# Performance work log

Hardware: AMD Instinct MI355X
Metric: run time of the kernel (lower is better)

## Reference

```python
import jax, jax.numpy as jnp
import numpy as np

B, N = 32, 25200          # batch, anchors (YOLOX @ 1280, strides 8/16/32)
NUM_CLASSES = 80
CH = 5 + NUM_CLASSES
CONF_THRE = 0.7
NMS_THRE = 0.45
TOPK = 512                # fixed pre-/post-NMS candidate budget (jit-static)
CLASS_OFFSET = 4096.0     # class-offset trick from the torch code


def setup_inputs() -> dict:
    key = jax.random.key(0)
    pred = jax.random.uniform(key, (B, N, CH), dtype=jnp.float32)
    # put box coords in pixel scale so IoU/NMS behaves realistically
    pred = pred.at[..., :4].multiply(640.0)
    return {"prediction": pred}


def _pairwise_iou(boxes):
    # boxes: [K, 4] xyxy -> iou: [K, K] (same math as torchvision.ops.nms)
    x1, y1, x2, y2 = boxes[:, 0], boxes[:, 1], boxes[:, 2], boxes[:, 3]
    area = (x2 - x1) * (y2 - y1)
    iw = jnp.clip(jnp.minimum(x2[:, None], x2[None, :]) - jnp.maximum(x1[:, None], x1[None, :]), 0.0)
    ih = jnp.clip(jnp.minimum(y2[:, None], y2[None, :]) - jnp.maximum(y1[:, None], y1[None, :]), 0.0)
    inter = iw * ih
    return inter / (area[:, None] + area[None, :] - inter)


def _greedy_nms(boxes, valid, iou_thre):
    # boxes are pre-sorted by descending score; greedy suppression identical to torchvision NMS
    iou = _pairwise_iou(boxes)  # [K, K]
    idx = jnp.arange(boxes.shape[0])

    def body(i, keep):
        suppress = (iou[i] > iou_thre) & (idx > i) & keep[i]
        return keep & ~suppress

    return jax.lax.fori_loop(0, boxes.shape[0], body, valid)


def _per_image(pred):
    # pred: [N, 5+C]
    cx, cy, w, h = pred[:, 0], pred[:, 1], pred[:, 2], pred[:, 3]
    hw, hh = w * 0.5, h * 0.5
    boxes = jnp.stack([cx - hw, cy - hh, cx + hw, cy + hh], axis=1)  # [N, 4] xyxy

    cls_scores = pred[:, 5:5 + NUM_CLASSES]
    class_conf = jnp.max(cls_scores, axis=1)
    class_pred = jnp.argmax(cls_scores, axis=1)
    conf = pred[:, 4] * class_conf                      # obj * class score
    valid = conf >= CONF_THRE

    # confidence filter + sort-by-score via fixed-size top-k (invalids ranked last)
    rank = jnp.where(valid, conf, -1.0)
    _, order = jax.lax.top_k(rank, TOPK)                # [TOPK], descending score
    b = boxes[order]
    c = conf[order]
    cl = class_pred[order]
    v = valid[order]

    nms_boxes = b + cl.astype(b.dtype)[:, None] * CLASS_OFFSET
    keep = _greedy_nms(nms_boxes, v, NMS_THRE)          # [TOPK] bool

    det = jnp.concatenate([b, c[:, None], cl.astype(jnp.float32)[:, None]], axis=1)  # [TOPK, 6]
    det = det * jax.lax.stop_gradient(keep.astype(det.dtype))[:, None]
    return det, keep


def reference(prediction):
    # returns padded detections [B, TOPK, 6] (x1,y1,x2,y2,conf,cls) and keep mask [B, TOPK]
    det, keep = jax.vmap(_per_image)(prediction)
    return det, keep
```

## Files before the change

kernel.cpp:

```cpp
#include <hip/hip_runtime.h>
#include <stdint.h>

#define BATCH 32
#define NANCH 25200
#define CH 85
#define NCLS 80
#define TOPK 512
#define CONF_THRE 0.7f
#define NMS_THRE 0.45f
#define CLS_OFF 4096.0f

typedef unsigned long long u64;
typedef unsigned int u32;

#define OFF_CONF  0
#define OFF_NMS   3225600
#define OFF_DET   3553280
#define OFF_VALID 3946496
#define OFF_MASK  3948544

__global__ __launch_bounds__(256) void scan_kernel(const float* __restrict__ pred,
                                                   u32* __restrict__ conf32) {
    const int tid = threadIdx.x;
    const int lane = tid & 63;
    const int wv = tid >> 6;
    const int g = lane >> 4;
    const int l = lane & 15;
    const int a = blockIdx.x * 16 + wv * 4 + g;
    const size_t base = (size_t)a * CH;

    float m = -1.0f, obj = 0.0f;
    {
        const float4 q = *(const float4*)(pred + base + (l << 2));
        const int p = l << 2;
        if (p + 0 >= 5) m = fmaxf(m, q.x); else if (p + 0 == 4) obj = q.x;
        if (p + 1 >= 5) m = fmaxf(m, q.y); else if (p + 1 == 4) obj = q.y;
        if (p + 2 >= 5) m = fmaxf(m, q.z); else if (p + 2 == 4) obj = q.z;
        if (p + 3 >= 5) m = fmaxf(m, q.w); else if (p + 3 == 4) obj = q.w;
    }
    if (l < 5) {
        const float4 q = *(const float4*)(pred + base + 64 + (l << 2));
        m = fmaxf(fmaxf(m, fmaxf(q.x, q.y)), fmaxf(q.z, q.w));
    } else if (l == 5) {
        m = fmaxf(m, pred[base + 84]);
    }
    #pragma unroll
    for (int off = 1; off < 16; off <<= 1) m = fmaxf(m, __shfl_xor(m, off));
    const float ob = __shfl(obj, (lane & 48) + 1);
    const float conf = ob * m;
    if (l == 0)
        conf32[a] = (conf >= CONF_THRE) ? __float_as_uint(conf) : 0u;
}

__global__ __launch_bounds__(1024) void select_kernel(const float* __restrict__ pred,
                                                      const u32* __restrict__ conf32,
                                                      float* __restrict__ nmsG,
                                                      float* __restrict__ detG,
                                                      u64* __restrict__ validG) {
    __shared__ u64 sbuf[1024];
    __shared__ u64 sorted[1024];
    __shared__ u32 hist[256];
    __shared__ u32 wtot[4];
    __shared__ u32 s_cnt, s_pivot;
    __shared__ unsigned char val[TOPK];

    const int img = blockIdx.x;
    const int tid = threadIdx.x;
    const int lane = tid & 63;
    const int wv = tid >> 6;

    if (tid == 0) { s_cnt = 0u; s_pivot = 0u; }
    if (tid < 256) hist[tid] = 0u;
    __syncthreads();

    const u32* cd = conf32 + (size_t)img * NANCH;
    for (int i = tid; i < NANCH; i += 1024) {
        const u32 c = cd[i];
        if (c) atomicAdd(&hist[(c >> 15) & 255u], 1u);
    }
    __syncthreads();

    u32 v = 0, s = 0;
    if (tid < 256) {
        v = hist[tid]; s = v;
        #pragma unroll
        for (int off = 1; off < 64; off <<= 1) {
            const u32 t = __shfl_down(s, off);
            if (lane + off < 64) s += t;
        }
        if (lane == 0) wtot[wv] = s;
    }
    __syncthreads();
    if (tid < 256) {
        u32 add = 0;
        for (int w2 = wv + 1; w2 < 4; ++w2) add += wtot[w2];
        const u32 sfull = s + add;
        const u32 snext = sfull - v;
        if (sfull >= TOPK && snext < TOPK) s_pivot = (u32)tid;
    }
    __syncthreads();
    const u32 T = 0x3F000000u | (s_pivot << 15);

    for (int i = tid; i < NANCH; i += 1024) {
        const u32 c = cd[i];
        if (c >= T) {
            const u32 pos = atomicAdd(&s_cnt, 1u);
            if (pos < 1024u)
                sbuf[pos] = ((u64)c << 32) | (u64)(0xFFFFFFFFu - (u32)i);
        }
    }
    __syncthreads();
    const u32 mc = (s_cnt > 1024u) ? 1024u : s_cnt;

    sorted[tid] = 0ull;
    u32 rank = 0; u64 my = 0ull;
    if (tid < (int)mc) {
        my = sbuf[tid];
        for (u32 i = 0; i < mc; ++i) rank += (sbuf[i] > my) ? 1u : 0u;
    }
    __syncthreads();
    if (tid < (int)mc && rank < 1024u) sorted[rank] = my;
    __syncthreads();

    const int g = lane >> 4;
    const int l = lane & 15;
    float* nb_ = nmsG + (size_t)img * (5 * TOPK);
    float* dt_ = detG + (size_t)img * (6 * TOPK);
    for (int pass = 0; pass < 8; ++pass) {
        const int r = pass * 64 + wv * 4 + g;
        const u64 key = sorted[r];
        const float conf = __uint_as_float((u32)(key >> 32));
        const bool okrow = conf >= CONF_THRE;
        float x1 = 0.f, y1 = 0.f, x2 = 0.f, y2 = 0.f, clsf = 0.f;
        float vv = -1.0f;
        int ci = l;
        if (okrow) {
            const u32 anchor = 0xFFFFFFFFu - (u32)(key & 0xFFFFFFFFull);
            const float* row = pred + ((size_t)img * NANCH + anchor) * CH;
            const float v0 = row[5 + l];
            const float v1 = row[21 + l];
            const float v2 = row[37 + l];
            const float v3 = row[53 + l];
            const float v4 = row[69 + l];
            float4 box;
            if (l == 0) box = *(const float4*)row;
            vv = v0; ci = l;
            if (v1 > vv) { vv = v1; ci = 16 + l; }
            if (v2 > vv) { vv = v2; ci = 32 + l; }
            if (v3 > vv) { vv = v3; ci = 48 + l; }
            if (v4 > vv) { vv = v4; ci = 64 + l; }
            #pragma unroll
            for (int off = 8; off > 0; off >>= 1) {
                const float ov = __shfl_xor(vv, off);
                const int oi = __shfl_xor(ci, off);
                if (ov > vv || (ov == vv && oi < ci)) { vv = ov; ci = oi; }
            }
            if (l == 0) {
                const float hw = box.z * 0.5f, hh = box.w * 0.5f;
                x1 = box.x - hw; y1 = box.y - hh; x2 = box.x + hw; y2 = box.y + hh;
                clsf = (float)ci;
            }
        }
        if (l == 0) {
            const float off = clsf * CLS_OFF;
            const float X1 = x1 + off, Y1 = y1 + off, X2 = x2 + off, Y2 = y2 + off;
            nb_[0 * TOPK + r] = X1; nb_[1 * TOPK + r] = Y1;
            nb_[2 * TOPK + r] = X2; nb_[3 * TOPK + r] = Y2;
            nb_[4 * TOPK + r] = (X2 - X1) * (Y2 - Y1);
            dt_[r * 6 + 0] = x1; dt_[r * 6 + 1] = y1;
            dt_[r * 6 + 2] = x2; dt_[r * 6 + 3] = y2;
            dt_[r * 6 + 4] = okrow ? conf : 0.0f;
            dt_[r * 6 + 5] = clsf;
            val[r] = okrow ? 1 : 0;
        }
    }
    __syncthreads();

    if (tid < TOPK) {
        const u64 vb = __ballot(val[tid] != 0);
        if (lane == 0) validG[img * 8 + wv] = vb;
    }
}

__global__ __launch_bounds__(256) void iou_kernel(const float* __restrict__ nmsG,
                                                  u64* __restrict__ maskG) {
    __shared__ float bx1[TOPK], by1[TOPK], bx2[TOPK], by2[TOPK], bar[TOPK];
    const int img = blockIdx.x;
    const int slab = blockIdx.y;
    const int tid = threadIdx.x;
    const int lane = tid & 63;
    const float* nb_ = nmsG + (size_t)img * (5 * TOPK);
    for (int i = tid; i < TOPK; i += 256) {
        bx1[i] = nb_[i];            by1[i] = nb_[TOPK + i];
        bx2[i] = nb_[2 * TOPK + i]; by2[i] = nb_[3 * TOPK + i];
        bar[i] = nb_[4 * TOPK + i];
    }
    __syncthreads();
    const int q0 = slab * (16 * TOPK);
    for (int q = q0 + tid; q < q0 + 16 * TOPK; q += 256) {
        const int i = q >> 9;
        const int j = q & (TOPK - 1);
        bool sup = false;
        if (j > i) {
            const float xx1 = fmaxf(bx1[i], bx1[j]);
            const float yy1 = fmaxf(by1[i], by1[j]);
            const float xx2 = fminf(bx2[i], bx2[j]);
            const float yy2 = fminf(by2[i], by2[j]);
            const float iw = fmaxf(xx2 - xx1, 0.0f);
            const float ih = fmaxf(yy2 - yy1, 0.0f);
            const float inter = iw * ih;
            const float uni = bar[i] + bar[j] - inter;
            const float iou = inter / uni;
            sup = iou > NMS_THRE;
        }
        const u64 bm = __ballot(sup);
        if (lane == 0) maskG[(size_t)img * 4096 + (q >> 6)] = bm;
    }
}

__global__ __launch_bounds__(256) void greedy_kernel(const u64* __restrict__ maskG,
                                                     const u64* __restrict__ validG,
                                                     const float* __restrict__ detG,
                                                     float* __restrict__ out) {
    __shared__ u64 m[TOPK * 8];
    __shared__ u64 kw8[8];
    const int img = blockIdx.x;
    const int tid = threadIdx.x;
    const int lane = tid & 63;
    const int wv = tid >> 6;
    const u64* mg = maskG + (size_t)img * 4096;
    for (int i = tid; i < 4096; i += 256) m[i] = mg[i];
    __syncthreads();

    if (wv == 0) {
        const bool ld = lane < 8;
        u64 kw = ld ? validG[img * 8 + lane] : 0ull;
        u64 p0 = ld ? m[0 * 8 + lane] : 0ull;
        u64 p1 = ld ? m[1 * 8 + lane] : 0ull;
        u64 p2 = ld ? m[2 * 8 + lane] : 0ull;
        u64 p3 = ld ? m[3 * 8 + lane] : 0ull;
        for (int i = 0; i < TOPK; i += 4) {
            {
                const u64 w = __shfl(kw, i >> 6);
                const u64 bit = (w >> (i & 63)) & 1ull;
                kw &= ~(p0 & (0ull - bit));
                p0 = (ld && i + 4 < TOPK) ? m[(i + 4) * 8 + lane] : 0ull;
            }
            {
                const u64 w = __shfl(kw, (i + 1) >> 6);
                const u64 bit = (w >> ((i + 1) & 63)) & 1ull;
                kw &= ~(p1 & (0ull - bit));
                p1 = (ld && i + 5 < TOPK) ? m[(i + 5) * 8 + lane] : 0ull;
            }
            {
                const u64 w = __shfl(kw, (i + 2) >> 6);
                const u64 bit = (w >> ((i + 2) & 63)) & 1ull;
                kw &= ~(p2 & (0ull - bit));
                p2 = (ld && i + 6 < TOPK) ? m[(i + 6) * 8 + lane] : 0ull;
            }
            {
                const u64 w = __shfl(kw, (i + 3) >> 6);
                const u64 bit = (w >> ((i + 3) & 63)) & 1ull;
                kw &= ~(p3 & (0ull - bit));
                p3 = (ld && i + 7 < TOPK) ? m[(i + 7) * 8 + lane] : 0ull;
            }
        }
        if (ld) kw8[lane] = kw;
    }
    __syncthreads();

    const float* dt_ = detG + (size_t)img * (6 * TOPK);
    float* det_out = out + (size_t)img * (TOPK * 6);
    float* keep_out = out + (size_t)BATCH * TOPK * 6 + (size_t)img * TOPK;
    for (int idx = tid; idx < TOPK * 6; idx += 256) {
        const int r = idx / 6;
        const float kf = ((kw8[r >> 6] >> (r & 63)) & 1ull) ? 1.0f : 0.0f;
        det_out[idx] = dt_[idx] * kf;
    }
    for (int r = tid; r < TOPK; r += 256) {
        keep_out[r] = ((kw8[r >> 6] >> (r & 63)) & 1ull) ? 1.0f : 0.0f;
    }
}

extern "C" void kernel_launch(void* const* d_in, const int* in_sizes, int n_in,
                              void* d_out, int out_size, void* d_ws, size_t ws_size,
                              hipStream_t stream) {
    const float* pred = (const float*)d_in[0];
    float* out = (float*)d_out;
    char* ws = (char*)d_ws;
    u32* conf32 = (u32*)(ws + OFF_CONF);
    float* nmsG = (float*)(ws + OFF_NMS);
    float* detG = (float*)(ws + OFF_DET);
    u64* validG = (u64*)(ws + OFF_VALID);
    u64* maskG = (u64*)(ws + OFF_MASK);

    scan_kernel<<<(BATCH * NANCH) / 16, 256, 0, stream>>>(pred, conf32);
    select_kernel<<<BATCH, 1024, 0, stream>>>(pred, conf32, nmsG, detG, validG);
    dim3 g4(BATCH, 32);
    iou_kernel<<<g4, 256, 0, stream>>>(nmsG, maskG);
    greedy_kernel<<<BATCH, 256, 0, stream>>>(maskG, validG, detG, out);
}
```

Measured before the change: 449.2 us.

## Compact passing anchors into per-image lists during scan, narrow class-argmax groups

The scan kernel now appends only the anchors that pass the confidence threshold to a per-image list, using a block-level ballot and one global atomic per block. The select kernel then builds its histogram and collects candidates from that short list instead of rereading all 25200 confidence words twice per image. This cuts the serial per-image work in the single-block select stage. It adds a zero kernel launch, an extra shared-memory barrier and global atomics in the scan, and makes the list order nondeterministic, though ties are still broken by anchor index. The class-argmax gather also moves from 16 lanes per row to 8 lanes per row, handling twice as many rows per pass.

```diff
diff --git a/kernel.cpp b/kernel.cpp
--- a/kernel.cpp
+++ b/kernel.cpp
@@ -13,14 +13,21 @@
 typedef unsigned long long u64;
 typedef unsigned int u32;
 
-#define OFF_CONF  0
-#define OFF_NMS   3225600
-#define OFF_DET   3553280
-#define OFF_VALID 3946496
-#define OFF_MASK  3948544
+#define OFF_LIST  0
+#define OFF_CNT   6451200
+#define OFF_NMS   6451456
+#define OFF_DET   6779136
+#define OFF_VALID 7172352
+#define OFF_MASK  7174400
+
+__global__ __launch_bounds__(64) void zero_kernel(u32* __restrict__ cntG) {
+    if (threadIdx.x < BATCH) cntG[threadIdx.x] = 0u;
+}
 
 __global__ __launch_bounds__(256) void scan_kernel(const float* __restrict__ pred,
-                                                   u32* __restrict__ conf32) {
+                                                   u64* __restrict__ listG,
+                                                   u32* __restrict__ cntG) {
+    __shared__ u32 sc[16];
     const int tid = threadIdx.x;
     const int lane = tid & 63;
     const int wv = tid >> 6;
@@ -49,11 +56,31 @@
     const float ob = __shfl(obj, (lane & 48) + 1);
     const float conf = ob * m;
     if (l == 0)
-        conf32[a] = (conf >= CONF_THRE) ? __float_as_uint(conf) : 0u;
+        sc[wv * 4 + g] = (conf >= CONF_THRE) ? __float_as_uint(conf) : 0u;
+    __syncthreads();
+
+    if (tid < 16) {
+        const u32 cc = sc[tid];
+        const u64 mask = __ballot(cc != 0u);
+        if (mask) {
+            const u32 n = __popc((u32)mask);
+            const u32 img = (u32)blockIdx.x / (NANCH / 16);
+            u32 bs = 0;
+            if (tid == 0) bs = atomicAdd(&cntG[img], n);
+            bs = __shfl(bs, 0);
+            if (cc) {
+                const u32 rnk = __popc((u32)mask & ((1u << tid) - 1u));
+                const u32 anchor = (u32)(blockIdx.x * 16 + tid) - img * NANCH;
+                listG[(size_t)img * NANCH + bs + rnk] =
+                    ((u64)cc << 32) | (u64)(0xFFFFFFFFu - anchor);
+            }
+        }
+    }
 }
 
 __global__ __launch_bounds__(1024) void select_kernel(const float* __restrict__ pred,
-                                                      const u32* __restrict__ conf32,
+                                                      const u64* __restrict__ listG,
+                                                      const u32* __restrict__ cntG,
                                                       float* __restrict__ nmsG,
                                                       float* __restrict__ detG,
                                                       u64* __restrict__ validG) {
@@ -73,10 +100,12 @@
     if (tid < 256) hist[tid] = 0u;
     __syncthreads();
 
-    const u32* cd = conf32 + (size_t)img * NANCH;
-    for (int i = tid; i < NANCH; i += 1024) {
-        const u32 c = cd[i];
-        if (c) atomicAdd(&hist[(c >> 15) & 255u], 1u);
+    const u32 cnt = cntG[img];
+    const u64* keys = listG + (size_t)img * NANCH;
+
+    for (u32 i = tid; i < cnt; i += 1024) {
+        const u32 c = (u32)(keys[i] >> 32);
+        atomicAdd(&hist[(c >> 15) & 255u], 1u);
     }
     __syncthreads();
 
@@ -101,12 +130,11 @@
     __syncthreads();
     const u32 T = 0x3F000000u | (s_pivot << 15);
 
-    for (int i = tid; i < NANCH; i += 1024) {
-        const u32 c = cd[i];
-        if (c >= T) {
+    for (u32 i = tid; i < cnt; i += 1024) {
+        const u64 k = keys[i];
+        if ((u32)(k >> 32) >= T) {
             const u32 pos = atomicAdd(&s_cnt, 1u);
-            if (pos < 1024u)
-                sbuf[pos] = ((u64)c << 32) | (u64)(0xFFFFFFFFu - (u32)i);
+            if (pos < 1024u) sbuf[pos] = k;
         }
     }
     __syncthreads();
@@ -122,35 +150,31 @@
     if (tid < (int)mc && rank < 1024u) sorted[rank] = my;
     __syncthreads();
 
-    const int g = lane >> 4;
-    const int l = lane & 15;
+    const int g = lane >> 3;
+    const int l = lane & 7;
     float* nb_ = nmsG + (size_t)img * (5 * TOPK);
     float* dt_ = detG + (size_t)img * (6 * TOPK);
-    for (int pass = 0; pass < 8; ++pass) {
-        const int r = pass * 64 + wv * 4 + g;
+    for (int pass = 0; pass < 4; ++pass) {
+        const int r = pass * 128 + wv * 8 + g;
         const u64 key = sorted[r];
         const float conf = __uint_as_float((u32)(key >> 32));
         const bool okrow = conf >= CONF_THRE;
         float x1 = 0.f, y1 = 0.f, x2 = 0.f, y2 = 0.f, clsf = 0.f;
-        float vv = -1.0f;
-        int ci = l;
         if (okrow) {
             const u32 anchor = 0xFFFFFFFFu - (u32)(key & 0xFFFFFFFFull);
             const float* row = pred + ((size_t)img * NANCH + anchor) * CH;
-            const float v0 = row[5 + l];
-            const float v1 = row[21 + l];
-            const float v2 = row[37 + l];
-            const float v3 = row[53 + l];
-            const float v4 = row[69 + l];
+            float vs[10];
+            #pragma unroll
+            for (int k = 0; k < 10; ++k) vs[k] = row[5 + l + 8 * k];
             float4 box;
             if (l == 0) box = *(const float4*)row;
-            vv = v0; ci = l;
-            if (v1 > vv) { vv = v1; ci = 16 + l; }
-            if (v2 > vv) { vv = v2; ci = 32 + l; }
-            if (v3 > vv) { vv = v3; ci = 48 + l; }
-            if (v4 > vv) { vv = v4; ci = 64 + l; }
+            float vv = vs[0];
+            int ci = l;
             #pragma unroll
-            for (int off = 8; off > 0; off >>= 1) {
+            for (int k = 1; k < 10; ++k)
+                if (vs[k] > vv) { vv = vs[k]; ci = 8 * k + l; }
+            #pragma unroll
+            for (int off = 4; off > 0; off >>= 1) {
                 const float ov = __shfl_xor(vv, off);
                 const int oi = __shfl_xor(ci, off);
                 if (ov > vv || (ov == vv && oi < ci)) { vv = ov; ci = oi; }
@@ -288,14 +312,16 @@
     const float* pred = (const float*)d_in[0];
     float* out = (float*)d_out;
     char* ws = (char*)d_ws;
-    u32* conf32 = (u32*)(ws + OFF_CONF);
+    u64* listG = (u64*)(ws + OFF_LIST);
+    u32* cntG = (u32*)(ws + OFF_CNT);
     float* nmsG = (float*)(ws + OFF_NMS);
     float* detG = (float*)(ws + OFF_DET);
     u64* validG = (u64*)(ws + OFF_VALID);
     u64* maskG = (u64*)(ws + OFF_MASK);
 
-    scan_kernel<<<(BATCH * NANCH) / 16, 256, 0, stream>>>(pred, conf32);
-    select_kernel<<<BATCH, 1024, 0, stream>>>(pred, conf32, nmsG, detG, validG);
+    zero_kernel<<<1, 64, 0, stream>>>(cntG);
+    scan_kernel<<<(BATCH * NANCH) / 16, 256, 0, stream>>>(pred, listG, cntG);
+    select_kernel<<<BATCH, 1024, 0, stream>>>(pred, listG, cntG, nmsG, detG, validG);
     dim3 g4(BATCH, 32);
     iou_kernel<<<g4, 256, 0, stream>>>(nmsG, maskG);
     greedy_kernel<<<BATCH, 256, 0, stream>>>(maskG, validG, detG, out);
```

Measured after the change: 910.3 us. 103% more time.
